# Optimization experiments

Measured on AMD Instinct MI355X. Metric: run time of the kernel, lower is better.

## Reference

```python
import jax, jax.numpy as jnp
import numpy as np

B, S, H = 2, 2048, 1024
NH, HD = 16, 64
WINDOW = 512
NEG = -10000.0


def setup_inputs() -> dict:
    key = jax.random.key(0)
    ks = jax.random.split(key, 8)
    sc = 0.02
    return {
        "hidden_states": jax.random.normal(ks[0], (B, S, H), dtype=jnp.float32),
        "attention_mask": jnp.zeros((B, 1, 1, S), dtype=jnp.float32),
        "Wq": jax.random.normal(ks[1], (H, H), dtype=jnp.float32) * sc,
        "bq": jnp.zeros((H,), dtype=jnp.float32),
        "Wk": jax.random.normal(ks[2], (H, H), dtype=jnp.float32) * sc,
        "bk": jnp.zeros((H,), dtype=jnp.float32),
        "Wv": jax.random.normal(ks[3], (H, H), dtype=jnp.float32) * sc,
        "bv": jnp.zeros((H,), dtype=jnp.float32),
    }


def _heads(x):
    # [b, t, (h d)] -> [b, h, t, d]
    b, t, _ = x.shape
    return x.reshape(b, t, NH, HD).transpose(0, 2, 1, 3)


def reference(hidden_states, attention_mask, Wq, bq, Wk, bk, Wv, bv):
    q = _heads(hidden_states @ Wq.T + bq)
    k = _heads(hidden_states @ Wk.T + bk)
    v = _heads(hidden_states @ Wv.T + bv)

    # Faithful mask construction (note: window mask is triu(diag=-WINDOW),
    # penalizing the recent window, exactly as in the source).
    i = jnp.arange(S)[:, None]
    j = jnp.arange(S)[None, :]
    causal_mask = jnp.where(j > i, NEG, 0.0).astype(jnp.float32)          # triu, diag=1
    window_mask = jnp.where(j >= i - WINDOW, NEG, 0.0).astype(jnp.float32)  # triu, diag=-512
    mask = causal_mask + window_mask + attention_mask  # [b,1,S,S]

    scale = 1.0 / jnp.sqrt(jnp.asarray(HD, dtype=q.dtype))
    scores = jnp.einsum("bhtd,bhsd->bhts", q, k) * scale + mask  # [b,h,S,S]
    probs = jax.nn.softmax(scores, axis=-1)
    out = jnp.einsum("bhts,bhsd->bhtd", probs, v)  # [b,h,S,d]
    # [b,h,t,d] -> [b,t,(h d)]
    return out.transpose(0, 2, 1, 3).reshape(B, S, H)
```

## Files before the change

kernel.cpp:

```cpp
#include <hip/hip_runtime.h>

typedef float f32x2 __attribute__((ext_vector_type(2)));
typedef float f32x4 __attribute__((ext_vector_type(4)));
typedef float f32x16 __attribute__((ext_vector_type(16)));
typedef _Float16 half8 __attribute__((ext_vector_type(8)));
typedef _Float16 half4 __attribute__((ext_vector_type(4)));
typedef unsigned int u32;
typedef u32 u32x4 __attribute__((ext_vector_type(4)));

#define S_LEN 2048
#define NHEAD 16
#define HDIM 64
#define BATCH 2
#define WINDOW 512
#define M2_FIX 5.770780163555852f
#define LOG2E 1.4426950408889634f

#define GLDS16(gp, lp) __builtin_amdgcn_global_load_lds( \
    (const __attribute__((address_space(1))) void*)(gp), \
    (__attribute__((address_space(3))) void*)(lp), 16, 0, 0)


__global__ __launch_bounds__(256) void convert_kernel(
    const float4* __restrict__ hs, const float4* __restrict__ wq,
    const float4* __restrict__ wk, const float4* __restrict__ wv,
    _Float16* __restrict__ hsb, _Float16* __restrict__ wb) {
  int i = blockIdx.x * 256 + threadIdx.x;
  float4 v;
  _Float16* dst;
  if (i < 1048576) {
    v = hs[i];
    dst = hsb + (size_t)i * 4;
  } else {
    int j = i - 1048576;
    if (j < 262144) v = wq[j];
    else if (j < 524288) v = wk[j - 262144];
    else v = wv[j - 524288];
    dst = wb + (size_t)j * 4;
  }
  half4 o;
  o[0] = (_Float16)v.x; o[1] = (_Float16)v.y;
  o[2] = (_Float16)v.z; o[3] = (_Float16)v.w;
  *(half4*)dst = o;
}

__global__ __launch_bounds__(512, 2) void qkv_gemm(
    const _Float16* __restrict__ A, const _Float16* __restrict__ W,
    const float* __restrict__ bq, const float* __restrict__ bk,
    const float* __restrict__ bv,
    _Float16* __restrict__ Qf, _Float16* __restrict__ Kf, _Float16* __restrict__ Vf) {
  __shared__ _Float16 sbuf[65536];
  const int tid = threadIdx.x;
  const int wv = tid >> 6;
  const int lane = tid & 63;
  const int g = lane >> 4;
  const int c = lane & 15;
  const int bid = blockIdx.x;
  const int m0 = (bid & 15) * 256;
  const int n0 = (bid >> 4) * 256;
  const int wm = wv >> 2;
  const int wn = wv & 3;

  const int srow = tid >> 3;
  const int sk = ((tid & 7) ^ ((tid >> 3) & 7)) * 8;
  const _Float16* aSrc = A + (size_t)(m0 + srow) * 1024 + sk;
  const _Float16* bSrc = W + (size_t)(n0 + srow) * 1024 + sk;
  char* const ldsB = (char*)&sbuf[0];

  auto STAGE_A = [&](int bf_, int k0, int grp) __attribute__((always_inline)) {
    GLDS16(aSrc + (size_t)grp * 65536 + k0,
           ldsB + bf_ * 32768 + grp * 8192 + tid * 16);
  };
  auto STAGE_B = [&](int bf_, int k0, int grp) __attribute__((always_inline)) {
    GLDS16(bSrc + (size_t)grp * 65536 + k0,
           ldsB + 65536 + bf_ * 32768 + grp * 8192 + tid * 16);
  };

  const int slot0 = ((0 * 4 + g) ^ (c & 7)) * 8;
  const int slot1 = ((1 * 4 + g) ^ (c & 7)) * 8;
  const int aRow = wm * 128 + c;
  const int bRow = wn * 64 + c;

  f32x4 acc[8][4];
#pragma unroll
  for (int i = 0; i < 8; ++i)
#pragma unroll
    for (int j = 0; j < 4; ++j) acc[i][j] = (f32x4){0.f, 0.f, 0.f, 0.f};

#pragma unroll
  for (int grp = 0; grp < 4; ++grp) STAGE_A(0, 0, grp);
#pragma unroll
  for (int grp = 0; grp < 4; ++grp) STAGE_B(0, 0, grp);
  asm volatile("s_waitcnt vmcnt(0)" ::: "memory");
  __builtin_amdgcn_sched_barrier(0);
  __builtin_amdgcn_s_barrier();

  half8 bfr[4][2];
  for (int t = 0; t < 16; ++t) {
    const int bf = t & 1;
    const int abase = bf * 16384;
    const int bbase = 32768 + bf * 16384;
    const int kn = (t + 1) * 64;
    const bool st = t < 15;

#pragma unroll
    for (int p = 0; p < 4; ++p) {
      if (st) {
        if (p == 0)      { STAGE_A(bf ^ 1, kn, 0); STAGE_A(bf ^ 1, kn, 1); }
        else if (p == 1) { STAGE_A(bf ^ 1, kn, 2); STAGE_A(bf ^ 1, kn, 3); }
        else if (p == 2) { STAGE_B(bf ^ 1, kn, 0); STAGE_B(bf ^ 1, kn, 1); }
        else             { STAGE_B(bf ^ 1, kn, 2); STAGE_B(bf ^ 1, kn, 3); }
      }
      if (p == 0) {
#pragma unroll
        for (int nf = 0; nf < 4; ++nf) {
          bfr[nf][0] = *(const half8*)&sbuf[bbase + (bRow + nf * 16) * 64 + slot0];
          bfr[nf][1] = *(const half8*)&sbuf[bbase + (bRow + nf * 16) * 64 + slot1];
        }
      }
      half8 aq[2][2];
#pragma unroll
      for (int mi = 0; mi < 2; ++mi) {
        const int row = aRow + (2 * p + mi) * 16;
        aq[mi][0] = *(const half8*)&sbuf[abase + row * 64 + slot0];
        aq[mi][1] = *(const half8*)&sbuf[abase + row * 64 + slot1];
      }
      asm volatile("s_waitcnt lgkmcnt(0)" ::: "memory");
      __builtin_amdgcn_sched_barrier(0);
      __builtin_amdgcn_s_setprio(1);
#pragma unroll
      for (int nf = 0; nf < 4; ++nf)
#pragma unroll
        for (int mi = 0; mi < 2; ++mi) {
          acc[2 * p + mi][nf] = __builtin_amdgcn_mfma_f32_16x16x32_f16(
              aq[mi][0], bfr[nf][0], acc[2 * p + mi][nf], 0, 0, 0);
          acc[2 * p + mi][nf] = __builtin_amdgcn_mfma_f32_16x16x32_f16(
              aq[mi][1], bfr[nf][1], acc[2 * p + mi][nf], 0, 0, 0);
        }
      __builtin_amdgcn_s_setprio(0);
      if (p == 3) {
        asm volatile("s_waitcnt vmcnt(0)" ::: "memory");
        __builtin_amdgcn_sched_barrier(0);
      }
      __builtin_amdgcn_s_barrier();
    }
  }

  const int nAbs = n0 + wn * 64;
  const int kind = nAbs >> 10;
  const int nb = nAbs & 1023;
  const int head = nb >> 6;
  const float* bias = kind == 0 ? bq : (kind == 1 ? bk : bv);
  _Float16* dst = kind == 0 ? Qf : (kind == 1 ? Kf : Vf);
  _Float16* ob = &sbuf[wv * 8192];

  if (kind < 2) {
    const float scl = kind == 0 ? (0.125f * LOG2E) : 1.0f;
#pragma unroll
    for (int nf = 0; nf < 4; ++nf) {
      const int d = nf * 16 + c;
      const float bsv = bias[nb + d];
      const int base = nf * 512 + ((c >> 3) & 1) * 256 + (c & 7);
#pragma unroll
      for (int mf = 0; mf < 8; ++mf) {
#pragma unroll
        for (int r = 0; r < 4; ++r) {
          ob[(mf >> 1) * 2048 + base + (mf & 1) * 128 + g * 32 + r * 8] =
              (_Float16)((acc[mf][nf][r] + bsv) * scl);
        }
      }
    }
  } else {
#pragma unroll
    for (int nf = 0; nf < 4; ++nf) {
      const int d = nf * 16 + c;
      const float bsv = bias[nb + d];
#pragma unroll
      for (int mf = 0; mf < 8; ++mf) {
        half4 v4;
#pragma unroll
        for (int r = 0; r < 4; ++r) v4[r] = (_Float16)(acc[mf][nf][r] + bsv);
        *(half4*)&ob[(mf >> 1) * 2048 + ((nf >> 1) * 2 + (mf & 1)) * 512 +
                     ((g >> 1) * 32 + (nf & 1) * 16 + c) * 8 + (g & 1) * 4] = v4;
      }
    }
  }

  const int mRow = m0 + wm * 128;
  const int bI = mRow >> 11;
  const size_t gbase = (size_t)(bI * NHEAD + head) * 131072 +
                       (size_t)((mRow & 2047) >> 5) * 2048;
#pragma unroll
  for (int i = 0; i < 16; ++i) {
    half8 v = *(const half8*)&ob[i * 512 + lane * 8];
    *(half8*)&dst[gbase + i * 512 + lane * 8] = v;
  }
}

__global__ __launch_bounds__(256) void attn_kernel(
    const _Float16* __restrict__ Qf, const _Float16* __restrict__ Kf,
    const _Float16* __restrict__ Vf, const float* __restrict__ amask,
    float* __restrict__ out) {
  __shared__ _Float16 obuf[4][32][72];
  __shared__ float lbuf[4][32];
  const int tid = threadIdx.x;
  const int w = tid >> 6;
  const int lane = tid & 63;
  const int q31 = lane & 31;
  const int h = lane >> 5;
  const int bid = blockIdx.x;
  const int bh = bid & 31;
  const int idx = 63 - (bid >> 5);
  const int i0 = idx * 32;
  const int bI = bh >> 4;
  const int head = bh & 15;

  const _Float16* Qh = Qf + (size_t)bh * 131072;
  const _Float16* Kh = Kf + (size_t)bh * 131072;
  const _Float16* Vh = Vf + (size_t)bh * 131072;
  const float* am = amask + (size_t)bI * S_LEN;

  const int q = i0 + q31;
  const int hiq = (q <= WINDOW) ? q : (q - WINDOW - 1);
  const int last = i0 + 31;
  const int himax = (last <= WINDOW) ? last
                    : ((i0 <= WINDOW) ? WINDOW : (last - WINDOW - 1));
  const int hiq_min = (last <= WINDOW) ? i0
                      : ((i0 > WINDOW) ? (i0 - WINDOW - 1) : 0);
  const int ntiles = (himax >> 5) + 1;
  const int nfull = (hiq_min + 1) >> 5;
  const int lim = hiq - 4 * h;

  half8 qf[4];
#pragma unroll
  for (int ch = 0; ch < 4; ++ch)
    qf[ch] = *(const half8*)&Qh[(size_t)idx * 2048 + ch * 512 + lane * 8];

  f32x16 zero16, m2init;
#pragma unroll
  for (int r = 0; r < 16; ++r) { zero16[r] = 0.f; m2init[r] = -M2_FIX; }
  f32x16 oacc0 = zero16, oacc1 = zero16;
  f32x2 lp[4];
#pragma unroll
  for (int r = 0; r < 4; ++r) lp[r] = (f32x2){0.f, 0.f};

  auto computeTile = [&](half8 k0, half8 k1, half8 k2, half8 k3,
                         half8 vf0, half8 vf1, half8 vf2, half8 vf3,
                         f32x4 am0, f32x4 am1, f32x4 am2, f32x4 am3, int t)
      __attribute__((always_inline)) {
    const int j0 = t * 32;
    f32x4 amv[4] = {am0, am1, am2, am3};

    __builtin_amdgcn_s_setprio(1);
    f32x16 st = __builtin_amdgcn_mfma_f32_32x32x16_f16(k0, qf[0], m2init, 0, 0, 0);
    st = __builtin_amdgcn_mfma_f32_32x32x16_f16(k1, qf[1], st, 0, 0, 0);
    st = __builtin_amdgcn_mfma_f32_32x32x16_f16(k2, qf[2], st, 0, 0, 0);
    st = __builtin_amdgcn_mfma_f32_32x32x16_f16(k3, qf[3], st, 0, 0, 0);
    __builtin_amdgcn_s_setprio(0);

    float p[16];
#pragma unroll
    for (int r = 0; r < 16; ++r)
      p[r] = __builtin_fmaf(amv[r >> 2][r & 3], LOG2E, st[r]);
    if (t >= nfull) {
      const int lm = lim - j0;
#pragma unroll
      for (int r = 0; r < 16; ++r) {
        const int off = (r & 3) + 8 * (r >> 2);
        p[r] = (off <= lm) ? p[r] : -3e38f;
      }
    }
#pragma unroll
    for (int r = 0; r < 16; ++r) p[r] = __builtin_amdgcn_exp2f(p[r]);
#pragma unroll
    for (int j = 0; j < 4; ++j) {
      lp[j] += (f32x2){p[2 * j], p[2 * j + 1]};
      lp[j] += (f32x2){p[8 + 2 * j], p[9 + 2 * j]};
    }

    u32 pk[8];
#pragma unroll
    for (int r = 0; r < 8; ++r) {
      auto c2 = __builtin_amdgcn_cvt_pkrtz(p[2 * r], p[2 * r + 1]);
      pk[r] = __builtin_bit_cast(u32, c2);
    }
    u32 a0 = pk[0], b0 = pk[2];
    u32 a1 = pk[1], b1 = pk[3];
    u32 a2 = pk[4], b2 = pk[6];
    u32 a3 = pk[5], b3 = pk[7];
    asm("v_permlane32_swap_b32 %0, %1" : "+v"(a0), "+v"(b0));
    asm("v_permlane32_swap_b32 %0, %1" : "+v"(a1), "+v"(b1));
    asm("v_permlane32_swap_b32 %0, %1" : "+v"(a2), "+v"(b2));
    asm("v_permlane32_swap_b32 %0, %1" : "+v"(a3), "+v"(b3));
    const half8 pf0 = __builtin_bit_cast(half8, (u32x4){a0, a1, b0, b1});
    const half8 pf1 = __builtin_bit_cast(half8, (u32x4){a2, a3, b2, b3});

    __builtin_amdgcn_s_setprio(1);
    oacc0 = __builtin_amdgcn_mfma_f32_32x32x16_f16(vf0, pf0, oacc0, 0, 0, 0);
    oacc0 = __builtin_amdgcn_mfma_f32_32x32x16_f16(vf1, pf1, oacc0, 0, 0, 0);
    oacc1 = __builtin_amdgcn_mfma_f32_32x32x16_f16(vf2, pf0, oacc1, 0, 0, 0);
    oacc1 = __builtin_amdgcn_mfma_f32_32x32x16_f16(vf3, pf1, oacc1, 0, 0, 0);
    __builtin_amdgcn_s_setprio(0);
  };

#define LOADALL(k0, k1, k2, k3, v0, v1, v2, v3, a0_, a1_, a2_, a3_, tt)  \
  {                                                                      \
    const _Float16* kt = Kh + (size_t)(tt) * 2048 + lane * 8;            \
    const _Float16* vt = Vh + (size_t)(tt) * 2048 + lane * 8;            \
    const float* at = am + (tt) * 32 + 4 * h;                            \
    k0 = *(const half8*)&kt[0];                                          \
    k1 = *(const half8*)&kt[512];                                        \
    k2 = *(const half8*)&kt[1024];                                       \
    k3 = *(const half8*)&kt[1536];                                       \
    v0 = *(const half8*)&vt[0];                                          \
    v1 = *(const half8*)&vt[512];                                        \
    v2 = *(const half8*)&vt[1024];                                       \
    v3 = *(const half8*)&vt[1536];                                       \
    a0_ = *(const f32x4*)&at[0];                                         \
    a1_ = *(const f32x4*)&at[8];                                         \
    a2_ = *(const f32x4*)&at[16];                                        \
    a3_ = *(const f32x4*)&at[24];                                        \
  }

  int t = w;
  if (t < ntiles) {
    half8 k0, k1, k2, k3, v0, v1, v2, v3;
    f32x4 a0, a1, a2, a3;
    LOADALL(k0, k1, k2, k3, v0, v1, v2, v3, a0, a1, a2, a3, t);
    int tn = t + 4;
    while (tn < ntiles) {
      half8 n0, n1, n2, n3, u0, u1, u2, u3;
      f32x4 e0, e1, e2, e3;
      LOADALL(n0, n1, n2, n3, u0, u1, u2, u3, e0, e1, e2, e3, tn);
      computeTile(k0, k1, k2, k3, v0, v1, v2, v3, a0, a1, a2, a3, t);
      k0 = n0; k1 = n1; k2 = n2; k3 = n3;
      v0 = u0; v1 = u1; v2 = u2; v3 = u3;
      a0 = e0; a1 = e1; a2 = e2; a3 = e3;
      t = tn;
      tn += 4;
    }
    computeTile(k0, k1, k2, k3, v0, v1, v2, v3, a0, a1, a2, a3, t);
  }

  f32x2 s2 = (lp[0] + lp[1]) + (lp[2] + lp[3]);
  float lw = s2[0] + s2[1];
  lw += __shfl_xor(lw, 32);
  if (h == 0) lbuf[w][q31] = lw;
#pragma unroll
  for (int j = 0; j < 4; ++j) {
    half4 h0, h1;
#pragma unroll
    for (int e = 0; e < 4; ++e) {
      h0[e] = (_Float16)oacc0[4 * j + e];
      h1[e] = (_Float16)oacc1[4 * j + e];
    }
    *(half4*)&obuf[w][q31][4 * h + 8 * j]      = h0;
    *(half4*)&obuf[w][q31][32 + 4 * h + 8 * j] = h1;
  }
  __syncthreads();

  const int mq = tid >> 3;
  const int md = (tid & 7) * 8;
  const float lt = (lbuf[0][mq] + lbuf[1][mq]) + (lbuf[2][mq] + lbuf[3][mq]);
  float s[8];
  half8 p0 = *(const half8*)&obuf[0][mq][md];
#pragma unroll
  for (int e = 0; e < 8; ++e) s[e] = (float)p0[e];
#pragma unroll
  for (int w4 = 1; w4 < 4; ++w4) {
    half8 pw = *(const half8*)&obuf[w4][mq][md];
#pragma unroll
    for (int e = 0; e < 8; ++e) s[e] += (float)pw[e];
  }
  const float inv = 1.0f / lt;
  float4 s0, s1;
  s0.x = s[0] * inv; s0.y = s[1] * inv; s0.z = s[2] * inv; s0.w = s[3] * inv;
  s1.x = s[4] * inv; s1.y = s[5] * inv; s1.z = s[6] * inv; s1.w = s[7] * inv;
  float* op = out + ((size_t)(bI * S_LEN + i0 + mq)) * 1024 + head * 64 + md;
  *(float4*)op = s0;
  *(float4*)(op + 4) = s1;
}

extern "C" void kernel_launch(void* const* d_in, const int* in_sizes, int n_in,
                              void* d_out, int out_size, void* d_ws, size_t ws_size,
                              hipStream_t stream) {
  const float* hs = (const float*)d_in[0];
  const float* am = (const float*)d_in[1];
  const float* Wq = (const float*)d_in[2];
  const float* bq = (const float*)d_in[3];
  const float* Wk = (const float*)d_in[4];
  const float* bk = (const float*)d_in[5];
  const float* Wv = (const float*)d_in[6];
  const float* bv = (const float*)d_in[7];
  float* out = (float*)d_out;

  char* ws = (char*)d_ws;
  _Float16* hsb = (_Float16*)(ws);
  _Float16* wb  = (_Float16*)(ws + 8388608);
  _Float16* Qf  = (_Float16*)(ws + 14680064);
  _Float16* Kf  = (_Float16*)(ws + 23068672);
  _Float16* Vf  = (_Float16*)(ws + 31457280);

  convert_kernel<<<7168, 256, 0, stream>>>(
      (const float4*)hs, (const float4*)Wq, (const float4*)Wk, (const float4*)Wv, hsb, wb);
  qkv_gemm<<<192, 512, 0, stream>>>(hsb, wb, bq, bk, bv, Qf, Kf, Vf);
  attn_kernel<<<2048, 256, 0, stream>>>(Qf, Kf, Vf, am, out);
}
```

Before: 74.37 us.

## Shrink QKV GEMM tiles to 128x128 to fill more CUs

The QKV projection GEMM drops from 256x256 output tiles to 128x128 tiles, raising the grid from 192 to 768 blocks and halving shared memory so more blocks fit per CU. The inner loop is restructured so each k-step issues the next tile's global-to-LDS loads between MFMA batches instead of across four phases. The epilogue is reworked to write half-head slabs in the same layout the attention kernel expects. Smaller tiles give better occupancy on a GPU with many CUs, at the cost of lower data reuse per block and more global traffic.

```diff
diff --git a/kernel.cpp b/kernel.cpp
--- a/kernel.cpp
+++ b/kernel.cpp
@@ -44,27 +44,26 @@
   *(half4*)dst = o;
 }
 
-__global__ __launch_bounds__(512, 2) void qkv_gemm(
+__global__ __launch_bounds__(512, 4) void qkv_gemm(
     const _Float16* __restrict__ A, const _Float16* __restrict__ W,
     const float* __restrict__ bq, const float* __restrict__ bk,
     const float* __restrict__ bv,
     _Float16* __restrict__ Qf, _Float16* __restrict__ Kf, _Float16* __restrict__ Vf) {
-  __shared__ _Float16 sbuf[65536];
+  __shared__ _Float16 sbuf[32768];
   const int tid = threadIdx.x;
   const int wv = tid >> 6;
   const int lane = tid & 63;
   const int g = lane >> 4;
   const int c = lane & 15;
   const int bid = blockIdx.x;
-  const int m0 = (bid & 15) * 256;
-  const int n0 = (bid >> 4) * 256;
+  const int m0 = (bid & 31) * 128;
+  const int n0 = (bid >> 5) * 128;
   const int wm = wv >> 2;
   const int wn = wv & 3;
 
-  const int srow = tid >> 3;
   const int sk = ((tid & 7) ^ ((tid >> 3) & 7)) * 8;
-  const _Float16* aSrc = A + (size_t)(m0 + srow) * 1024 + sk;
-  const _Float16* bSrc = W + (size_t)(n0 + srow) * 1024 + sk;
+  const _Float16* aSrc = A + (size_t)(m0 + (tid >> 3)) * 1024 + sk;
+  const _Float16* bSrc = W + (size_t)(n0 + (tid >> 3)) * 1024 + sk;
   char* const ldsB = (char*)&sbuf[0];
 
   auto STAGE_A = [&](int bf_, int k0, int grp) __attribute__((always_inline)) {
@@ -73,128 +72,127 @@
   };
   auto STAGE_B = [&](int bf_, int k0, int grp) __attribute__((always_inline)) {
     GLDS16(bSrc + (size_t)grp * 65536 + k0,
-           ldsB + 65536 + bf_ * 32768 + grp * 8192 + tid * 16);
+           ldsB + bf_ * 32768 + 16384 + grp * 8192 + tid * 16);
   };
 
-  const int slot0 = ((0 * 4 + g) ^ (c & 7)) * 8;
-  const int slot1 = ((1 * 4 + g) ^ (c & 7)) * 8;
-  const int aRow = wm * 128 + c;
-  const int bRow = wn * 64 + c;
-
-  f32x4 acc[8][4];
-#pragma unroll
-  for (int i = 0; i < 8; ++i)
-#pragma unroll
-    for (int j = 0; j < 4; ++j) acc[i][j] = (f32x4){0.f, 0.f, 0.f, 0.f};
-
-#pragma unroll
-  for (int grp = 0; grp < 4; ++grp) STAGE_A(0, 0, grp);
-#pragma unroll
-  for (int grp = 0; grp < 4; ++grp) STAGE_B(0, 0, grp);
+  const int slot0 = ((g) ^ (c & 7)) * 8;
+  const int slot1 = ((4 + g) ^ (c & 7)) * 8;
+  const int aRow = wm * 64 + c;
+  const int bRow = wn * 32 + c;
+
+  f32x4 acc[4][2];
+#pragma unroll
+  for (int i = 0; i < 4; ++i)
+#pragma unroll
+    for (int j = 0; j < 2; ++j) acc[i][j] = (f32x4){0.f, 0.f, 0.f, 0.f};
+
+  STAGE_A(0, 0, 0); STAGE_A(0, 0, 1);
+  STAGE_B(0, 0, 0); STAGE_B(0, 0, 1);
   asm volatile("s_waitcnt vmcnt(0)" ::: "memory");
   __builtin_amdgcn_sched_barrier(0);
   __builtin_amdgcn_s_barrier();
 
-  half8 bfr[4][2];
+  half8 bfr[2][2], af[4][2];
   for (int t = 0; t < 16; ++t) {
     const int bf = t & 1;
     const int abase = bf * 16384;
-    const int bbase = 32768 + bf * 16384;
+    const int bbase = bf * 16384 + 8192;
     const int kn = (t + 1) * 64;
     const bool st = t < 15;
 
 #pragma unroll
-    for (int p = 0; p < 4; ++p) {
-      if (st) {
-        if (p == 0)      { STAGE_A(bf ^ 1, kn, 0); STAGE_A(bf ^ 1, kn, 1); }
-        else if (p == 1) { STAGE_A(bf ^ 1, kn, 2); STAGE_A(bf ^ 1, kn, 3); }
-        else if (p == 2) { STAGE_B(bf ^ 1, kn, 0); STAGE_B(bf ^ 1, kn, 1); }
-        else             { STAGE_B(bf ^ 1, kn, 2); STAGE_B(bf ^ 1, kn, 3); }
+    for (int nf = 0; nf < 2; ++nf) {
+      bfr[nf][0] = *(const half8*)&sbuf[bbase + (bRow + nf * 16) * 64 + slot0];
+      bfr[nf][1] = *(const half8*)&sbuf[bbase + (bRow + nf * 16) * 64 + slot1];
+    }
+#pragma unroll
+    for (int mf = 0; mf < 2; ++mf) {
+      const int row = aRow + mf * 16;
+      af[mf][0] = *(const half8*)&sbuf[abase + row * 64 + slot0];
+      af[mf][1] = *(const half8*)&sbuf[abase + row * 64 + slot1];
+    }
+    if (st) { STAGE_A(bf ^ 1, kn, 0); STAGE_A(bf ^ 1, kn, 1); }
+#pragma unroll
+    for (int mf = 2; mf < 4; ++mf) {
+      const int row = aRow + mf * 16;
+      af[mf][0] = *(const half8*)&sbuf[abase + row * 64 + slot0];
+      af[mf][1] = *(const half8*)&sbuf[abase + row * 64 + slot1];
+    }
+    __builtin_amdgcn_s_setprio(1);
+#pragma unroll
+    for (int nf = 0; nf < 2; ++nf)
+#pragma unroll
+      for (int mf = 0; mf < 2; ++mf) {
+        acc[mf][nf] = __builtin_amdgcn_mfma_f32_16x16x32_f16(af[mf][0], bfr[nf][0], acc[mf][nf], 0, 0, 0);
+        acc[mf][nf] = __builtin_amdgcn_mfma_f32_16x16x32_f16(af[mf][1], bfr[nf][1], acc[mf][nf], 0, 0, 0);
       }
-      if (p == 0) {
-#pragma unroll
-        for (int nf = 0; nf < 4; ++nf) {
-          bfr[nf][0] = *(const half8*)&sbuf[bbase + (bRow + nf * 16) * 64 + slot0];
-          bfr[nf][1] = *(const half8*)&sbuf[bbase + (bRow + nf * 16) * 64 + slot1];
-        }
+    __builtin_amdgcn_s_setprio(0);
+    if (st) { STAGE_B(bf ^ 1, kn, 0); STAGE_B(bf ^ 1, kn, 1); }
+    __builtin_amdgcn_s_setprio(1);
+#pragma unroll
+    for (int nf = 0; nf < 2; ++nf)
+#pragma unroll
+      for (int mf = 2; mf < 4; ++mf) {
+        acc[mf][nf] = __builtin_amdgcn_mfma_f32_16x16x32_f16(af[mf][0], bfr[nf][0], acc[mf][nf], 0, 0, 0);
+        acc[mf][nf] = __builtin_amdgcn_mfma_f32_16x16x32_f16(af[mf][1], bfr[nf][1], acc[mf][nf], 0, 0, 0);
       }
-      half8 aq[2][2];
-#pragma unroll
-      for (int mi = 0; mi < 2; ++mi) {
-        const int row = aRow + (2 * p + mi) * 16;
-        aq[mi][0] = *(const half8*)&sbuf[abase + row * 64 + slot0];
-        aq[mi][1] = *(const half8*)&sbuf[abase + row * 64 + slot1];
-      }
-      asm volatile("s_waitcnt lgkmcnt(0)" ::: "memory");
-      __builtin_amdgcn_sched_barrier(0);
-      __builtin_amdgcn_s_setprio(1);
-#pragma unroll
-      for (int nf = 0; nf < 4; ++nf)
-#pragma unroll
-        for (int mi = 0; mi < 2; ++mi) {
-          acc[2 * p + mi][nf] = __builtin_amdgcn_mfma_f32_16x16x32_f16(
-              aq[mi][0], bfr[nf][0], acc[2 * p + mi][nf], 0, 0, 0);
-          acc[2 * p + mi][nf] = __builtin_amdgcn_mfma_f32_16x16x32_f16(
-              aq[mi][1], bfr[nf][1], acc[2 * p + mi][nf], 0, 0, 0);
-        }
-      __builtin_amdgcn_s_setprio(0);
-      if (p == 3) {
-        asm volatile("s_waitcnt vmcnt(0)" ::: "memory");
-        __builtin_amdgcn_sched_barrier(0);
-      }
-      __builtin_amdgcn_s_barrier();
-    }
-  }
-
-  const int nAbs = n0 + wn * 64;
+    __builtin_amdgcn_s_setprio(0);
+
+    asm volatile("s_waitcnt vmcnt(0)" ::: "memory");
+    __builtin_amdgcn_sched_barrier(0);
+    __builtin_amdgcn_s_barrier();
+  }
+
+  const int nAbs = n0 + wn * 32;
   const int kind = nAbs >> 10;
   const int nb = nAbs & 1023;
-  const int head = nb >> 6;
+  const int head = (nb >> 6) & 15;
+  const int halfsel = wn & 1;
   const float* bias = kind == 0 ? bq : (kind == 1 ? bk : bv);
   _Float16* dst = kind == 0 ? Qf : (kind == 1 ? Kf : Vf);
-  _Float16* ob = &sbuf[wv * 8192];
+  _Float16* ob = &sbuf[wv * 2048];
 
   if (kind < 2) {
     const float scl = kind == 0 ? (0.125f * LOG2E) : 1.0f;
 #pragma unroll
-    for (int nf = 0; nf < 4; ++nf) {
-      const int d = nf * 16 + c;
-      const float bsv = bias[nb + d];
-      const int base = nf * 512 + ((c >> 3) & 1) * 256 + (c & 7);
-#pragma unroll
-      for (int mf = 0; mf < 8; ++mf) {
+    for (int nf = 0; nf < 2; ++nf) {
+      const float bsv = bias[nb + nf * 16 + c];
+#pragma unroll
+      for (int mf = 0; mf < 4; ++mf) {
 #pragma unroll
         for (int r = 0; r < 4; ++r) {
-          ob[(mf >> 1) * 2048 + base + (mf & 1) * 128 + g * 32 + r * 8] =
+          ob[(mf >> 1) * 1024 + nf * 512 + ((c >> 3) & 1) * 256 +
+             ((mf & 1) * 16 + g * 4 + r) * 8 + (c & 7)] =
               (_Float16)((acc[mf][nf][r] + bsv) * scl);
         }
       }
     }
   } else {
 #pragma unroll
-    for (int nf = 0; nf < 4; ++nf) {
-      const int d = nf * 16 + c;
-      const float bsv = bias[nb + d];
-#pragma unroll
-      for (int mf = 0; mf < 8; ++mf) {
+    for (int nf = 0; nf < 2; ++nf) {
+      const float bsv = bias[nb + nf * 16 + c];
+#pragma unroll
+      for (int mf = 0; mf < 4; ++mf) {
         half4 v4;
 #pragma unroll
         for (int r = 0; r < 4; ++r) v4[r] = (_Float16)(acc[mf][nf][r] + bsv);
-        *(half4*)&ob[(mf >> 1) * 2048 + ((nf >> 1) * 2 + (mf & 1)) * 512 +
-                     ((g >> 1) * 32 + (nf & 1) * 16 + c) * 8 + (g & 1) * 4] = v4;
+        *(half4*)&ob[(mf >> 1) * 1024 + (mf & 1) * 512 + (g >> 1) * 256 +
+                     (nf * 16 + c) * 8 + (g & 1) * 4] = v4;
       }
     }
   }
 
-  const int mRow = m0 + wm * 128;
+  const int mRow = m0 + wm * 64;
   const int bI = mRow >> 11;
   const size_t gbase = (size_t)(bI * NHEAD + head) * 131072 +
-                       (size_t)((mRow & 2047) >> 5) * 2048;
-#pragma unroll
-  for (int i = 0; i < 16; ++i) {
-    half8 v = *(const half8*)&ob[i * 512 + lane * 8];
-    *(half8*)&dst[gbase + i * 512 + lane * 8] = v;
-  }
+                       (size_t)((mRow & 2047) >> 5) * 2048 + halfsel * 1024;
+#pragma unroll
+  for (int st2 = 0; st2 < 2; ++st2)
+#pragma unroll
+    for (int i2 = 0; i2 < 2; ++i2) {
+      half8 v = *(const half8*)&ob[st2 * 1024 + i2 * 512 + lane * 8];
+      *(half8*)&dst[gbase + st2 * 2048 + i2 * 512 + lane * 8] = v;
+    }
 }
 
 __global__ __launch_bounds__(256) void attn_kernel(
@@ -236,10 +234,10 @@
   for (int ch = 0; ch < 4; ++ch)
     qf[ch] = *(const half8*)&Qh[(size_t)idx * 2048 + ch * 512 + lane * 8];
 
-  f32x16 zero16, m2init;
-#pragma unroll
-  for (int r = 0; r < 16; ++r) { zero16[r] = 0.f; m2init[r] = -M2_FIX; }
-  f32x16 oacc0 = zero16, oacc1 = zero16;
+  f32x16 m2init;
+#pragma unroll
+  for (int r = 0; r < 16; ++r) m2init[r] = -M2_FIX;
+  f32x16 oacc0 = {}, oacc1 = {};
   f32x2 lp[4];
 #pragma unroll
   for (int r = 0; r < 4; ++r) lp[r] = (f32x2){0.f, 0.f};
@@ -403,6 +401,6 @@
 
   convert_kernel<<<7168, 256, 0, stream>>>(
       (const float4*)hs, (const float4*)Wq, (const float4*)Wk, (const float4*)Wv, hsb, wb);
-  qkv_gemm<<<192, 512, 0, stream>>>(hsb, wb, bq, bk, bv, Qf, Kf, Vf);
+  qkv_gemm<<<768, 512, 0, stream>>>(hsb, wb, bq, bk, bv, Qf, Kf, Vf);
   attn_kernel<<<2048, 256, 0, stream>>>(Qf, Kf, Vf, am, out);
 }
```

Measured after the change: 75.50 us. No clear change (+1.5%).
